# Kernel optimization log

Hardware: AMD Instinct MI355X
Metric: run time of the kernel (lower is better)

Reference implementation:

```python
import jax, jax.numpy as jnp
import numpy as np

# graph structure constants
G = 64            # num graphs
NPG = 1600        # nodes per graph
N = G * NPG       # 102400 total nodes
EPG = 51200       # edges per graph (avg degree 32)
E = G * EPG       # 3276800 total edges
F_IN = 512
H_OUT = 512
RATIO = 0.8
K = int(np.ceil(RATIO * NPG))   # 1280 kept nodes per graph
NK = G * K


def gcn_conv(x, src, dst, W, b, n, ew):
    """PyG GCNConv: D^-1/2 (A+I) D^-1/2 X W + b, with edge weights ew."""
    h = x @ W
    deg = jax.ops.segment_sum(ew, dst, num_segments=n) + 1.0  # +1 for self loop
    dis = jax.lax.rsqrt(deg)
    norm = dis[src] * dis[dst] * ew                 # [E]
    agg = jax.ops.segment_sum(h[src] * norm[:, None], dst, num_segments=n)
    return agg + h * (dis * dis)[:, None] + b       # self-loop norm = dis_i^2


def setup_inputs() -> dict:
    key = jax.random.key(0)
    k_x, k_e, k_w1, k_wr, k_wo, k_w2 = jax.random.split(key, 6)
    x = jax.random.normal(k_x, (N, F_IN), dtype=jnp.float32)
    # within-graph random edges
    local = jax.random.randint(k_e, (2, G, EPG), 0, NPG, dtype=jnp.int32)
    offs = (jnp.arange(G, dtype=jnp.int32) * NPG)[None, :, None]
    edge_index = (local + offs).reshape(2, E)
    batch = jnp.repeat(jnp.arange(G, dtype=jnp.int32), NPG)
    W1 = jax.random.normal(k_w1, (F_IN, 16), dtype=jnp.float32) * (1.0 / np.sqrt(F_IN))
    b1 = jnp.zeros((16,), jnp.float32)
    Wrel = jax.random.normal(k_wr, (16, 1), dtype=jnp.float32) * 0.25
    brel = jnp.zeros((1,), jnp.float32)
    Wroot = jax.random.normal(k_wo, (16, 1), dtype=jnp.float32) * 0.25
    W2 = jax.random.normal(k_w2, (16, H_OUT), dtype=jnp.float32) * 0.25
    b2 = jnp.zeros((H_OUT,), jnp.float32)
    return {"x": x, "edge_index": edge_index, "batch": batch,
            "W1": W1, "b1": b1, "Wrel": Wrel, "brel": brel,
            "Wroot": Wroot, "W2": W2, "b2": b2}


def reference(x, edge_index, batch, W1, b1, Wrel, brel, Wroot, W2, b2):
    src, dst = edge_index[0], edge_index[1]
    ones_e = jnp.ones((E,), x.dtype)
    # conv1 + relu
    h1 = jax.nn.relu(gcn_conv(x, src, dst, W1, b1, N, ones_e))   # [N,16]
    # SAGPooling score: GraphConv(16,1) = lin_rel(sum_j x_j) + lin_root(x), then tanh
    agg = jax.ops.segment_sum(h1[src], dst, num_segments=N)
    score = jnp.tanh((agg @ Wrel + brel + h1 @ Wroot)[:, 0])      # [N]
    # per-graph top-k (graphs are equal-sized, contiguous)
    vals, idx = jax.lax.top_k(score.reshape(G, NPG), K)           # [G,K]
    perm = (idx + (jnp.arange(G, dtype=idx.dtype) * NPG)[:, None]).reshape(-1)  # [NK]
    xk = h1[perm] * vals.reshape(-1)[:, None]                     # x[perm] * score[perm]
    # filter_adj: keep edges with both endpoints kept, remap indices
    kept = jnp.zeros((N,), bool).at[perm].set(True)
    inv = jnp.zeros((N,), jnp.int32).at[perm].set(jnp.arange(NK, dtype=jnp.int32))
    em = (kept[src] & kept[dst]).astype(x.dtype)                  # weight-0 == dropped edge
    # conv2 + relu on pooled graph
    h2 = jax.nn.relu(gcn_conv(xk, inv[src], inv[dst], W2, b2, NK, em))  # [NK,H]
    # global mean pool (each graph keeps exactly K nodes)
    out = jax.ops.segment_sum(h2, batch[perm], num_segments=G) / K
    return out
```

## Files before the change

### kernel.cpp

```cpp
#include <hip/hip_runtime.h>
#include <math.h>

#define G_    64
#define NPG_  1600
#define N_    (G_*NPG_)
#define EPG_  51200
#define E_    (G_*EPG_)
#define FIN_  512
#define HOUT_ 512
#define KEEP_ 1280

typedef _Float16 f16x8 __attribute__((ext_vector_type(8)));
typedef float f32x4 __attribute__((ext_vector_type(4)));
#define WSTR_ 520

union BXShared {
  struct {
    unsigned short csrs[EPG_];
    int hist[NPG_];
    int wsum[16];
  } b;
  struct {
    _Float16 wls[2][16][WSTR_];
  } x;
};

__global__ __launch_bounds__(1024, 4) void k_bx(
    const int* __restrict__ esrc, const int* __restrict__ edst,
    int* __restrict__ offs, int* __restrict__ rend,
    float* __restrict__ dis, unsigned short* __restrict__ csr,
    const float* __restrict__ x, const float* __restrict__ W1,
    float* __restrict__ hd) {
  __shared__ BXShared sm;
  const int t = threadIdx.x;
  const int lane = t & 63, wid = t >> 6;

  if (blockIdx.x < 64) {
    const int g = blockIdx.x;
    const int eb = g * EPG_, nb = g * NPG_;

    for (int i = t; i < NPG_; i += 1024) sm.b.hist[i] = 0;
    __syncthreads();
    for (int e = t; e < EPG_; e += 1024)
      atomicAdd(&sm.b.hist[edst[eb + e] - nb], 1);
    __syncthreads();

    int c0 = 0, c1 = 0;
    if (t < 800) { c0 = sm.b.hist[2 * t]; c1 = sm.b.hist[2 * t + 1]; }
    const int val = c0 + c1;
    int incl = val;
#pragma unroll
    for (int m = 1; m < 64; m <<= 1) {
      const int u = __shfl_up(incl, m);
      if (lane >= m) incl += u;
    }
    if (lane == 63) sm.b.wsum[wid] = incl;
    __syncthreads();
    int woff = 0;
    for (int w2 = 0; w2 < wid; ++w2) woff += sm.b.wsum[w2];
    incl += woff;
    if (t < 800) {
      const int excl = incl - val;
      const int p0 = excl, p1 = p0 + c0;
      offs[nb + 2 * t] = eb + p0;     rend[nb + 2 * t] = eb + p1;
      offs[nb + 2 * t + 1] = eb + p1; rend[nb + 2 * t + 1] = eb + p1 + c1;
      dis[nb + 2 * t] = rsqrtf((float)c0 + 1.0f);
      dis[nb + 2 * t + 1] = rsqrtf((float)c1 + 1.0f);
      sm.b.hist[2 * t] = p0;
      sm.b.hist[2 * t + 1] = p1;
    }
    __syncthreads();
    for (int e = t; e < EPG_; e += 1024) {
      const int s = esrc[eb + e];
      const int d = edst[eb + e] - nb;
      const int p = atomicAdd(&sm.b.hist[d], 1);
      sm.b.csrs[p] = (unsigned short)(s - nb);
    }
    __syncthreads();
    const uint4* s4 = reinterpret_cast<const uint4*>(sm.b.csrs);
    uint4* d4 = reinterpret_cast<uint4*>(csr + eb);
    for (int i = t; i < EPG_ / 8; i += 1024) d4[i] = s4[i];
  } else {
    for (int i = t; i < FIN_ * 16; i += 1024) {
      const int k = i >> 4, n = i & 15;
      const float w = W1[i];
      const _Float16 w1 = (_Float16)w;
      const float r = w - (float)w1;
      sm.x.wls[0][n][k] = w1;
      sm.x.wls[1][n][k] = (_Float16)r;
    }
    __syncthreads();

    const int g = lane >> 4, m = lane & 15;
    const int tile = (blockIdx.x - 64) * 16 + wid;
    const int rb = tile * 16;

    const float* xrow = x + (size_t)(rb + m) * FIN_ + g * 8;
    const _Float16* wb1 = &sm.x.wls[0][m][g * 8];
    const _Float16* wb2 = &sm.x.wls[1][m][g * 8];

    f32x4 acc = {0.f, 0.f, 0.f, 0.f};
#pragma unroll
    for (int t4 = 0; t4 < 16; ++t4) {
      const float4 p0 = *reinterpret_cast<const float4*>(xrow + t4 * 32);
      const float4 p1 = *reinterpret_cast<const float4*>(xrow + t4 * 32 + 4);
      const float xv[8] = {p0.x, p0.y, p0.z, p0.w, p1.x, p1.y, p1.z, p1.w};
      f16x8 a1, a2;
#pragma unroll
      for (int j = 0; j < 8; ++j) {
        const _Float16 h = (_Float16)xv[j];
        a1[j] = h;
        a2[j] = (_Float16)(xv[j] - (float)h);
      }
      const f16x8 b1 = *reinterpret_cast<const f16x8*>(wb1 + t4 * 32);
      const f16x8 b2 = *reinterpret_cast<const f16x8*>(wb2 + t4 * 32);
      acc = __builtin_amdgcn_mfma_f32_16x16x32_f16(a1, b1, acc, 0, 0, 0);
      acc = __builtin_amdgcn_mfma_f32_16x16x32_f16(a1, b2, acc, 0, 0, 0);
      acc = __builtin_amdgcn_mfma_f32_16x16x32_f16(a2, b1, acc, 0, 0, 0);
    }

#pragma unroll
    for (int rg = 0; rg < 4; ++rg)
      hd[(size_t)(rb + g * 4 + rg) * 16 + m] = acc[rg];
  }
}

__global__ __launch_bounds__(1024) void k_conv1l(
    const unsigned short* __restrict__ csr, const int* __restrict__ offs,
    const int* __restrict__ rend, const float* __restrict__ hd,
    const float* __restrict__ dis, const float* __restrict__ b1,
    const float* __restrict__ Wrel, const float* __restrict__ Wroot,
    float* __restrict__ h1, float* __restrict__ rarr, float* __restrict__ tarr) {
  __shared__ float hds[NPG_ * 16];
  const int g = blockIdx.x >> 2, q = blockIdx.x & 3;
  const int nb = g * NPG_;
  const int t = threadIdx.x;
  {
    const float4* src = reinterpret_cast<const float4*>(hd + (size_t)nb * 16);
    float4* dst = reinterpret_cast<float4*>(hds);
    for (int i = t; i < NPG_ * 4; i += 1024) {
      const float4 v = src[i];
      const float dd = dis[nb + (i >> 2)];
      dst[i] = make_float4(v.x * dd, v.y * dd, v.z * dd, v.w * dd);
    }
  }
  __syncthreads();
  const int c = t & 15;
  const float bb = b1[c], wr = Wrel[c], wo = Wroot[c];
  const int vend = q * 400 + 400;
  for (int vl = q * 400 + (t >> 4); vl < vend; vl += 64) {
    const int v = nb + vl;
    const int rs = offs[v], re = rend[v];
    float acc = 0.f;
    int k = rs;
    for (; k + 4 <= re; k += 4) {
      const int s0 = csr[k], s1 = csr[k + 1];
      const int s2 = csr[k + 2], s3 = csr[k + 3];
      acc += hds[s0 * 16 + c] + hds[s1 * 16 + c];
      acc += hds[s2 * 16 + c] + hds[s3 * 16 + c];
    }
    for (; k < re; ++k) acc += hds[csr[k] * 16 + c];
    const float dd = dis[v];
    float val = fmaf(acc + hds[vl * 16 + c], dd, bb);
    val = fmaxf(val, 0.f);
    h1[(size_t)v * 16 + c] = val;
    float r = val * wr;
    float tt = val * wo;
#pragma unroll
    for (int m = 1; m < 16; m <<= 1) {
      r += __shfl_xor(r, m);
      tt += __shfl_xor(tt, m);
    }
    if (c == 0) { rarr[v] = r; tarr[v] = tt; }
  }
}

__global__ __launch_bounds__(320) void k_score(
    const unsigned short* __restrict__ csr, const int* __restrict__ offs,
    const int* __restrict__ rend, const float* __restrict__ rarr,
    const float* __restrict__ tarr, const float* __restrict__ brel,
    float* __restrict__ scoreg, unsigned* __restrict__ uug) {
  __shared__ float rar[NPG_];
  const int g = blockIdx.x / 5, q = blockIdx.x % 5;
  const int nb = g * NPG_;
  const int t = threadIdx.x;
  for (int i = t; i < NPG_; i += 320) rar[i] = rarr[nb + i];
  __syncthreads();
  const int vl = q * 320 + t;
  const int v = nb + vl;
  const int rs = offs[v], re = rend[v];
  float sum = 0.f;
  int k = rs;
  for (; k + 4 <= re; k += 4) {
    sum += rar[csr[k]] + rar[csr[k + 1]];
    sum += rar[csr[k + 2]] + rar[csr[k + 3]];
  }
  for (; k < re; ++k) sum += rar[csr[k]];
  const float s = tanhf(sum + brel[0] + tarr[v]);
  scoreg[v] = s;
  const unsigned ub = __float_as_uint(s);
  uug[v] = (ub & 0x80000000u) ? ~ub : (ub | 0x80000000u);
}

__global__ __launch_bounds__(1024) void k_topk(
    const unsigned* __restrict__ uug, int* __restrict__ kept,
    float* __restrict__ out) {
  __shared__ unsigned uu[NPG_];
  __shared__ int kp[NPG_];
  __shared__ int hist[256];
  __shared__ int part[16];
  __shared__ int scal[2];
  const int g = blockIdx.x, t = threadIdx.x;
  const int lane = t & 63, wid = t >> 6;
  const int nb = g * NPG_;

  for (int i = t; i < NPG_; i += 1024) uu[i] = uug[nb + i];
  if (t == 0) { scal[0] = 0; scal[1] = KEEP_; }
  __syncthreads();

  const unsigned maskTab[4] = {0u, 0xFF000000u, 0xFFFF0000u, 0xFFFFFF00u};
  const int shTab[4] = {24, 16, 8, 0};
  for (int pass = 0; pass < 4; ++pass) {
    const unsigned lo = (unsigned)scal[0];
    const int remc = scal[1];
    const unsigned msk = maskTab[pass];
    const int sh = shTab[pass];
    if (t < 256) hist[t] = 0;
    __syncthreads();
    for (int v = t; v < NPG_; v += 1024) {
      const unsigned u = uu[v];
      if (((u ^ lo) & msk) == 0) atomicAdd(&hist[(u >> sh) & 255], 1);
    }
    __syncthreads();
    int hv = 0;
    if (t < 256) hv = hist[t];
    int incl = hv;
#pragma unroll
    for (int m = 1; m < 64; m <<= 1) {
      const int u2 = __shfl_up(incl, m);
      if (lane >= m) incl += u2;
    }
    if (t < 256 && lane == 63) part[wid] = incl;
    __syncthreads();
    if (t < 256) {
      int woff = 0;
      for (int w2 = 0; w2 < wid; ++w2) woff += part[w2];
      const int tot = part[0] + part[1] + part[2] + part[3];
      const int sb = tot - (incl + woff) + hv;
      const int sb1 = sb - hv;
      if (sb >= remc && sb1 < remc) {
        scal[0] = (int)(lo | ((unsigned)t << sh));
        scal[1] = remc - sb1;
      }
    }
    __syncthreads();
  }
  const unsigned T = (unsigned)scal[0];
  const int remT = scal[1];

  const int i0 = 2 * t, i1 = 2 * t + 1;
  int f0 = 0, f1 = 0;
  if (i0 < NPG_) f0 = (uu[i0] == T);
  if (i1 < NPG_) f1 = (uu[i1] == T);
  int incl2 = f0 + f1;
#pragma unroll
  for (int m = 1; m < 64; m <<= 1) {
    const int u2 = __shfl_up(incl2, m);
    if (lane >= m) incl2 += u2;
  }
  if (lane == 63) part[wid] = incl2;
  __syncthreads();
  int woff2 = 0;
  for (int w2 = 0; w2 < wid; ++w2) woff2 += part[w2];
  const int excl = incl2 + woff2 - (f0 + f1);
  if (i0 < NPG_) kp[i0] = (uu[i0] > T) || (f0 && excl < remT);
  if (i1 < NPG_) kp[i1] = (uu[i1] > T) || (f1 && (excl + f0) < remT);
  __syncthreads();
  for (int v = t; v < NPG_; v += 1024) kept[nb + v] = kp[v];
  if (t < HOUT_) out[g * HOUT_ + t] = 0.f;
}

__global__ __launch_bounds__(320) void k_post(
    const unsigned short* __restrict__ csr, const int* __restrict__ offs,
    const int* __restrict__ rend, const int* __restrict__ kept,
    const float* __restrict__ scoreg, const float* __restrict__ h1,
    float* __restrict__ dis2, float* __restrict__ h1w) {
  __shared__ int kp[NPG_];
  __shared__ float wvs[320];
  const int g = blockIdx.x / 5, q = blockIdx.x % 5;
  const int nb = g * NPG_;
  const int t = threadIdx.x;
  for (int i = t; i < NPG_; i += 320) kp[i] = kept[nb + i];
  __syncthreads();
  const int vl = q * 320 + t;
  const int v = nb + vl;
  float w = 0.f;
  if (kp[vl]) {
    const int rs = offs[v], re = rend[v];
    int c2 = 0, k = rs;
    for (; k + 4 <= re; k += 4) {
      c2 += kp[csr[k]] + kp[csr[k + 1]];
      c2 += kp[csr[k + 2]] + kp[csr[k + 3]];
    }
    for (; k < re; ++k) c2 += kp[csr[k]];
    const float d2 = rsqrtf((float)c2 + 1.0f);
    dis2[v] = d2;
    w = scoreg[v] * d2;
  }
  wvs[t] = w;
  __syncthreads();
  const size_t base = (size_t)(nb + q * 320) * 16;
  for (int i = t; i < 320 * 16; i += 320)
    h1w[base + i] = h1[base + i] * wvs[i >> 4];
}

__global__ __launch_bounds__(1024) void k_conv2l(
    const unsigned short* __restrict__ csr, const int* __restrict__ offs,
    const int* __restrict__ rend, const float* __restrict__ h1w,
    const int* __restrict__ kept, const float* __restrict__ dis2,
    float* __restrict__ y16) {
  __shared__ float hds[NPG_ * 16];
  const int g = blockIdx.x >> 2, q = blockIdx.x & 3;
  const int nb = g * NPG_;
  const int t = threadIdx.x;
  {
    const float4* src = reinterpret_cast<const float4*>(h1w + (size_t)nb * 16);
    float4* dst = reinterpret_cast<float4*>(hds);
    for (int i = t; i < NPG_ * 4; i += 1024) dst[i] = src[i];
  }
  __syncthreads();
  const int c = t & 15;
  const int vend = q * 400 + 400;
  for (int vl = q * 400 + (t >> 4); vl < vend; vl += 64) {
    const int v = nb + vl;
    if (!kept[v]) continue;
    const int rs = offs[v], re = rend[v];
    float acc = 0.f;
    int k = rs;
    for (; k + 4 <= re; k += 4) {
      const int s0 = csr[k], s1 = csr[k + 1];
      const int s2 = csr[k + 2], s3 = csr[k + 3];
      acc += hds[s0 * 16 + c] + hds[s1 * 16 + c];
      acc += hds[s2 * 16 + c] + hds[s3 * 16 + c];
    }
    for (; k < re; ++k) acc += hds[csr[k] * 16 + c];
    acc += hds[vl * 16 + c];
    y16[(size_t)v * 16 + c] = acc * dis2[v];
  }
}

__global__ __launch_bounds__(256, 1) void k_gemm2pool(const float* __restrict__ y16,
                                                      const int* __restrict__ kept,
                                                      const float* __restrict__ W2,
                                                      const float* __restrict__ b2,
                                                      float* __restrict__ out) {
  __shared__ float red[256];
  const int blk = blockIdx.x;
  const int g = blk >> 5;
  const int sub = blk & 31;
  const int jbase = (sub & 1) * 256;
  const int nstart = g * NPG_ + (sub >> 1) * 100;
  const int tid = threadIdx.x;
  const int wave = tid >> 6, lane = tid & 63;

  float w[16][4];
#pragma unroll
  for (int k = 0; k < 16; ++k)
#pragma unroll
    for (int c = 0; c < 4; ++c)
      w[k][c] = W2[k * HOUT_ + jbase + lane + c * 64];
  float b2r[4];
#pragma unroll
  for (int c = 0; c < 4; ++c) b2r[c] = b2[jbase + lane + c * 64];

  float acc[4] = {0.f, 0.f, 0.f, 0.f};
  for (int i = wave; i < 100; i += 4) {
    const int v = nstart + i;
    if (!kept[v]) continue;
    const float4* yp = reinterpret_cast<const float4*>(y16 + (size_t)v * 16);
    float4 q0 = yp[0], q1 = yp[1], q2 = yp[2], q3 = yp[3];
    const float yv[16] = {q0.x, q0.y, q0.z, q0.w, q1.x, q1.y, q1.z, q1.w,
                          q2.x, q2.y, q2.z, q2.w, q3.x, q3.y, q3.z, q3.w};
    float z[4] = {b2r[0], b2r[1], b2r[2], b2r[3]};
#pragma unroll
    for (int k = 0; k < 16; ++k)
#pragma unroll
      for (int c = 0; c < 4; ++c)
        z[c] = fmaf(yv[k], w[k][c], z[c]);
#pragma unroll
    for (int c = 0; c < 4; ++c) acc[c] += fmaxf(z[c], 0.f);
  }

  red[tid] = 0.f;
  __syncthreads();
#pragma unroll
  for (int c = 0; c < 4; ++c) atomicAdd(&red[lane + 64 * c], acc[c]);
  __syncthreads();
  atomicAdd(&out[g * HOUT_ + jbase + tid], red[tid] * (1.0f / (float)KEEP_));
}

extern "C" void kernel_launch(void* const* d_in, const int* in_sizes, int n_in,
                              void* d_out, int out_size, void* d_ws, size_t ws_size,
                              hipStream_t stream) {
  (void)in_sizes; (void)n_in; (void)out_size; (void)ws_size;
  const float* x     = (const float*)d_in[0];
  const int*   ei    = (const int*)  d_in[1];
  const float* W1    = (const float*)d_in[3];
  const float* b1    = (const float*)d_in[4];
  const float* Wrel  = (const float*)d_in[5];
  const float* brel  = (const float*)d_in[6];
  const float* Wroot = (const float*)d_in[7];
  const float* W2    = (const float*)d_in[8];
  const float* b2    = (const float*)d_in[9];
  const int* esrc = ei;
  const int* edst = ei + E_;

  char* ws = (char*)d_ws;
  float*          hd     = (float*)(ws);
  unsigned*       uug    = (unsigned*)(ws);
  float*          scoreg = (float*)(ws + 409600);
  float*          h1     = (float*)(ws + 6553600);
  float*          h1w    = (float*)(ws + 13107200);
  float*          y16    = (float*)(ws + 19660800);
  unsigned short* csr    = (unsigned short*)(ws + 26214400);
  int*            offs   = (int*)(ws + 32768000);
  int*            rendp  = (int*)(ws + 33177600);
  float*          dis    = (float*)(ws + 33587200);
  int*            kept   = (int*)(ws + 33996800);
  float*          rarr   = (float*)(ws + 34406400);
  float*          tarr   = (float*)(ws + 34816000);
  float*          dis2   = (float*)(ws + 35225600);
  float*          out    = (float*)d_out;

  hipLaunchKernelGGL(k_bx,        dim3(464),   dim3(1024), 0, stream,
                     esrc, edst, offs, rendp, dis, csr, x, W1, hd);
  hipLaunchKernelGGL(k_conv1l,    dim3(256),   dim3(1024), 0, stream,
                     csr, offs, rendp, hd, dis, b1, Wrel, Wroot, h1, rarr, tarr);
  hipLaunchKernelGGL(k_score,     dim3(320),   dim3(320),  0, stream,
                     csr, offs, rendp, rarr, tarr, brel, scoreg, uug);
  hipLaunchKernelGGL(k_topk,      dim3(G_),    dim3(1024), 0, stream,
                     uug, kept, out);
  hipLaunchKernelGGL(k_post,      dim3(320),   dim3(320),  0, stream,
                     csr, offs, rendp, kept, scoreg, h1, dis2, h1w);
  hipLaunchKernelGGL(k_conv2l,    dim3(256),   dim3(1024), 0, stream,
                     csr, offs, rendp, h1w, kept, dis2, y16);
  hipLaunchKernelGGL(k_gemm2pool, dim3(2048),  dim3(256),  0, stream,
                     y16, kept, W2, b2, out);
}
```

Baseline: 186.1 us.

## Use split-fp16 MFMA for W2 projection and pooling in gemm2pool

Rewrites the final projection-plus-mean-pool kernel to use 16x16x32 fp16 MFMA instructions. Both activations and W2 are split into high and low fp16 parts so the product keeps close to fp32 accuracy, with W2 staged transposed in shared memory. The grid becomes 256 blocks of 512 threads, each handling 400 nodes and accumulating all 512 outputs in registers. This replaces scalar FMA work, at the cost of heavy register use (128 accumulators), fewer blocks, and a small precision risk from the split-fp16 scheme.

```diff
diff --git a/kernel.cpp b/kernel.cpp
--- a/kernel.cpp
+++ b/kernel.cpp
@@ -349,54 +349,93 @@
   }
 }
 
-__global__ __launch_bounds__(256, 1) void k_gemm2pool(const float* __restrict__ y16,
-                                                      const int* __restrict__ kept,
-                                                      const float* __restrict__ W2,
-                                                      const float* __restrict__ b2,
-                                                      float* __restrict__ out) {
-  __shared__ float red[256];
-  const int blk = blockIdx.x;
-  const int g = blk >> 5;
-  const int sub = blk & 31;
-  const int jbase = (sub & 1) * 256;
-  const int nstart = g * NPG_ + (sub >> 1) * 100;
+__global__ __launch_bounds__(512, 1) void k_gemm2pool(
+    const float* __restrict__ y16, const int* __restrict__ kept,
+    const float* __restrict__ W2, const float* __restrict__ b2,
+    float* __restrict__ out) {
+  __shared__ _Float16 wt[2][HOUT_][16];
+  __shared__ float b2s[HOUT_];
+  __shared__ float red[HOUT_];
   const int tid = threadIdx.x;
-  const int wave = tid >> 6, lane = tid & 63;
-
-  float w[16][4];
-#pragma unroll
-  for (int k = 0; k < 16; ++k)
-#pragma unroll
-    for (int c = 0; c < 4; ++c)
-      w[k][c] = W2[k * HOUT_ + jbase + lane + c * 64];
-  float b2r[4];
-#pragma unroll
-  for (int c = 0; c < 4; ++c) b2r[c] = b2[jbase + lane + c * 64];
-
-  float acc[4] = {0.f, 0.f, 0.f, 0.f};
-  for (int i = wave; i < 100; i += 4) {
-    const int v = nstart + i;
-    if (!kept[v]) continue;
-    const float4* yp = reinterpret_cast<const float4*>(y16 + (size_t)v * 16);
-    float4 q0 = yp[0], q1 = yp[1], q2 = yp[2], q3 = yp[3];
-    const float yv[16] = {q0.x, q0.y, q0.z, q0.w, q1.x, q1.y, q1.z, q1.w,
-                          q2.x, q2.y, q2.z, q2.w, q3.x, q3.y, q3.z, q3.w};
-    float z[4] = {b2r[0], b2r[1], b2r[2], b2r[3]};
-#pragma unroll
-    for (int k = 0; k < 16; ++k)
-#pragma unroll
-      for (int c = 0; c < 4; ++c)
-        z[c] = fmaf(yv[k], w[k][c], z[c]);
-#pragma unroll
-    for (int c = 0; c < 4; ++c) acc[c] += fmaxf(z[c], 0.f);
-  }
-
-  red[tid] = 0.f;
-  __syncthreads();
-#pragma unroll
-  for (int c = 0; c < 4; ++c) atomicAdd(&red[lane + 64 * c], acc[c]);
-  __syncthreads();
-  atomicAdd(&out[g * HOUT_ + jbase + tid], red[tid] * (1.0f / (float)KEEP_));
+
+  for (int i = tid; i < 16 * HOUT_; i += 512) {
+    const int j = i & 511;
+    const int k = i >> 9;
+    const float w = W2[i];
+    const _Float16 w1 = (_Float16)w;
+    wt[0][j][k] = w1;
+    wt[1][j][k] = (_Float16)(w - (float)w1);
+  }
+  for (int i = tid; i < HOUT_; i += 512) { b2s[i] = b2[i]; red[i] = 0.f; }
+  __syncthreads();
+
+  const int g = blockIdx.x >> 2, q = blockIdx.x & 3;
+  const int nb = g * NPG_ + q * 400;
+  const int lane = tid & 63, wid = tid >> 6;
+  const int gg = lane >> 4, m = lane & 15;
+
+  float accv[32][4];
+#pragma unroll
+  for (int jt = 0; jt < 32; ++jt)
+#pragma unroll
+    for (int r = 0; r < 4; ++r) accv[jt][r] = 0.f;
+
+  for (int tt = wid; tt < 25; tt += 8) {
+    const int base = nb + tt * 16;
+    const int k0 = (gg & 1) * 8;
+    const float* yr = y16 + (size_t)(base + m) * 16 + k0;
+    float4 pa = make_float4(0.f, 0.f, 0.f, 0.f);
+    float4 pb = make_float4(0.f, 0.f, 0.f, 0.f);
+    if (kept[base + m]) {
+      pa = *reinterpret_cast<const float4*>(yr);
+      pb = *reinterpret_cast<const float4*>(yr + 4);
+    }
+    const float yv[8] = {pa.x, pa.y, pa.z, pa.w, pb.x, pb.y, pb.z, pb.w};
+    f16x8 y1, y2;
+#pragma unroll
+    for (int jj = 0; jj < 8; ++jj) {
+      const _Float16 h = (_Float16)yv[jj];
+      y1[jj] = h;
+      y2[jj] = (_Float16)(yv[jj] - (float)h);
+    }
+    const f16x8 A1 = (gg < 2) ? y1 : y2;
+    const f16x8 A2 = y1;
+    float km[4];
+#pragma unroll
+    for (int r = 0; r < 4; ++r)
+      km[r] = kept[base + gg * 4 + r] ? 1.f : 0.f;
+
+#pragma unroll 4
+    for (int jt = 0; jt < 32; ++jt) {
+      const int j = jt * 16 + m;
+      const f16x8 B1 = *reinterpret_cast<const f16x8*>(&wt[0][j][(gg & 1) * 8]);
+      f16x8 B2 = {0, 0, 0, 0, 0, 0, 0, 0};
+      if (gg < 2) B2 = *reinterpret_cast<const f16x8*>(&wt[1][j][gg * 8]);
+      f32x4 d = {0.f, 0.f, 0.f, 0.f};
+      d = __builtin_amdgcn_mfma_f32_16x16x32_f16(A1, B1, d, 0, 0, 0);
+      d = __builtin_amdgcn_mfma_f32_16x16x32_f16(A2, B2, d, 0, 0, 0);
+      const float bj = b2s[j];
+#pragma unroll
+      for (int r = 0; r < 4; ++r)
+        accv[jt][r] += km[r] * fmaxf(d[r] + bj, 0.f);
+    }
+  }
+
+#pragma unroll
+  for (int jt = 0; jt < 32; ++jt) {
+    float s = accv[jt][0] + accv[jt][1] + accv[jt][2] + accv[jt][3];
+    s += __shfl_xor(s, 16);
+    s += __shfl_xor(s, 32);
+    accv[jt][0] = s;
+  }
+  if (lane < 16) {
+#pragma unroll
+    for (int jt = 0; jt < 32; ++jt)
+      atomicAdd(&red[jt * 16 + lane], accv[jt][0]);
+  }
+  __syncthreads();
+  for (int i = tid; i < HOUT_; i += 512)
+    atomicAdd(&out[g * HOUT_ + i], red[i] * (1.0f / (float)KEEP_));
 }
 
 extern "C" void kernel_launch(void* const* d_in, const int* in_sizes, int n_in,
@@ -444,6 +483,6 @@
                      csr, offs, rendp, kept, scoreg, h1, dis2, h1w);
   hipLaunchKernelGGL(k_conv2l,    dim3(256),   dim3(1024), 0, stream,
                      csr, offs, rendp, h1w, kept, dis2, y16);
-  hipLaunchKernelGGL(k_gemm2pool, dim3(2048),  dim3(256),  0, stream,
+  hipLaunchKernelGGL(k_gemm2pool, dim3(256),   dim3(512),  0, stream,
                      y16, kept, W2, b2, out);
 }
```

After: 251.3 us. +35.0%, slower.
